# Kernel optimization log

Hardware: AMD Instinct MI355X
Metric: run time of the kernel (lower is better)

Reference implementation:

```python
import jax, jax.numpy as jnp
import numpy as np

EPS = 1e-5


def _prelu(x, a):
    return jnp.where(x >= 0, x, a * x)


def _chan_ln(x, gamma, beta, axis):
    # LayerNormalization4D: normalize over the channel axis, affine per channel
    mu = jnp.mean(x, axis=axis, keepdims=True)
    var = jnp.var(x, axis=axis, keepdims=True)
    return (x - mu) / jnp.sqrt(var + EPS) * gamma + beta


def setup_inputs() -> dict:
    key = jax.random.key(0)
    ks = jax.random.split(key, 12)
    B, C, T, F = 2, 64, 3000, 65
    H, D = 4, 4            # n_head, hid_chan
    E = C // H             # per-head value channels
    s = lambda k, shape: (jax.random.normal(k, shape, jnp.float32) * 0.05)
    return dict(
        x=jax.random.normal(ks[0], (B, C, T, F), jnp.float32),
        # per-head 1x1-conv Q/K/V projections (stacked over head axis)
        Wq=s(ks[1], (H, D, C)), bq=s(ks[2], (H, D)),
        aq=jnp.full((H,), 0.25, jnp.float32),
        gq=jnp.ones((H, D), jnp.float32), betaq=jnp.zeros((H, D), jnp.float32),
        Wk=s(ks[3], (H, D, C)), bk=s(ks[4], (H, D)),
        ak=jnp.full((H,), 0.25, jnp.float32),
        gk=jnp.ones((H, D), jnp.float32), betak=jnp.zeros((H, D), jnp.float32),
        Wv=s(ks[5], (H, E, C)), bv=s(ks[6], (H, E)),
        av=jnp.full((H,), 0.25, jnp.float32),
        gv=jnp.ones((H, E), jnp.float32), betav=jnp.zeros((H, E), jnp.float32),
        # final concat 1x1-conv projection
        Wp=s(ks[7], (C, C)), bp=s(ks[8], (C,)),
        ap=jnp.asarray(0.25, jnp.float32),
        gp=jnp.ones((C,), jnp.float32), betap=jnp.zeros((C,), jnp.float32),
    )


def _conv_act_norm_heads(x, W, b, a, g, beta):
    # x: [B,C,T,F]; W: [H,O,C] -> y: [B,H,O,T,F]
    y = jnp.einsum('hoc,bctf->bhotf', W, x) + b[None, :, :, None, None]
    y = _prelu(y, a[None, :, None, None, None])
    return _chan_ln(y, g[None, :, :, None, None], beta[None, :, :, None, None], axis=2)


def reference(x, Wq, bq, aq, gq, betaq, Wk, bk, ak, gk, betak,
              Wv, bv, av, gv, betav, Wp, bp, ap, gp, betap):
    B, C, T, F = x.shape
    H = Wq.shape[0]
    D = Wq.shape[1]
    E = Wv.shape[1]

    q = _conv_act_norm_heads(x, Wq, bq, aq, gq, betaq)   # [B,H,D,T,F]
    k = _conv_act_norm_heads(x, Wk, bk, ak, gk, betak)   # [B,H,D,T,F]
    v = _conv_act_norm_heads(x, Wv, bv, av, gv, betav)   # [B,H,E,T,F]

    # flatten (chan, freq) -> embedding per time step
    Qf = q.transpose(0, 1, 3, 2, 4).reshape(B, H, T, D * F)
    Kf = k.transpose(0, 1, 3, 2, 4).reshape(B, H, T, D * F)
    Vf = v.transpose(0, 1, 3, 2, 4).reshape(B, H, T, E * F)

    scale = 1.0 / jnp.sqrt(jnp.asarray(D * F, x.dtype))
    attn = jax.nn.softmax(jnp.einsum('bhtd,bhsd->bhts', Qf, Kf) * scale, axis=-1)
    o = jnp.einsum('bhts,bhse->bhte', attn, Vf)          # [B,H,T,E*F]

    # un-flatten and concat heads along channel dim
    o = o.reshape(B, H, T, E, F).transpose(0, 1, 3, 2, 4).reshape(B, H * E, T, F)

    # final 1x1 conv + PReLU + channel LN, then residual
    y = jnp.einsum('oc,bctf->botf', Wp, o) + bp[None, :, None, None]
    y = _prelu(y, ap)
    y = _chan_ln(y, gp[None, :, None, None], betap[None, :, None, None], axis=1)
    return y + x
```

## Files before the change

### kernel.cpp

```cpp
#include <hip/hip_runtime.h>
#include <stdint.h>

#define B_ 2
#define C_ 64
#define T_ 3000
#define F_ 65
#define H_ 4
#define D_ 4
#define E_ 16
#define TF_ (T_*F_)
#define NPT (B_*TF_)
#define EF 1040
#define TP 3072
#define TK 3008
#define DQK 260
#define SQK 328
#define VTROWS 1152
#define ABUF 8192
#define BBUF 4096

typedef unsigned short u16;
typedef unsigned int   u32;
typedef __attribute__((ext_vector_type(8))) short  s16x8;
typedef __attribute__((ext_vector_type(4))) float  f32x4;
typedef __attribute__((ext_vector_type(4))) u32    u32x4;

__device__ __forceinline__ float bf2f(u16 u){ return __uint_as_float(((u32)u)<<16); }
__device__ __forceinline__ float bf2f_lo(u32 u){ return __uint_as_float(u<<16); }
__device__ __forceinline__ float bf2f_hi(u32 u){ return __uint_as_float(u & 0xffff0000u); }
__device__ __forceinline__ u16 f2bf(float f){
  u32 u = __float_as_uint(f);
  u32 r = u + 0x7fffu + ((u>>16)&1u);
  return (u16)(r>>16);
}

__device__ __forceinline__ void gld16(const u16* g, u16* l){
  __builtin_amdgcn_global_load_lds((const __attribute__((address_space(1))) u32*)g,
                                   (__attribute__((address_space(3))) u32*)l,
                                   16, 0, 0);
}

__global__ __launch_bounds__(256) void qkv_kernel(
    const float* __restrict__ x,
    const float* __restrict__ Wq, const float* __restrict__ bq, const float* __restrict__ aq,
    const float* __restrict__ gq, const float* __restrict__ bteq,
    const float* __restrict__ Wk, const float* __restrict__ bk, const float* __restrict__ ak,
    const float* __restrict__ gk, const float* __restrict__ btek,
    const float* __restrict__ Wv, const float* __restrict__ bv, const float* __restrict__ av,
    const float* __restrict__ gv, const float* __restrict__ btev,
    u16* __restrict__ Qf, u16* __restrict__ Kf, u16* __restrict__ Vf,
    float* __restrict__ lbuf)
{
  __shared__ __align__(16) u16 wlds[2*96*64];
  const int tid = threadIdx.x;
  for (int i = tid; i < 6144; i += 256){
    const int row = i >> 6, c = i & 63;
    float w;
    if (row < 16)      w = Wq[row*64 + c];
    else if (row < 32) w = Wk[(row-16)*64 + c];
    else               w = Wv[(row-32)*64 + c];
    const u16 hi = f2bf(w);
    const u16 lo = f2bf(w - bf2f(hi));
    const int byo = ((row<<7) + (c<<1)) ^ ((row&7)<<4);
    *(u16*)((char*)wlds + byo)         = hi;
    *(u16*)((char*)wlds + 12288 + byo) = lo;
  }
  const int gid = blockIdx.x*256 + tid;
  if (gid < 8*TP) lbuf[gid] = 0.f;
  __syncthreads();

  const int wv_ = tid >> 6, l = tid & 63;
  const int lm = l & 15, lq = l >> 4;
  const int p0 = blockIdx.x*128 + wv_*32;

  int bb[2], rr[2]; bool ok[2];
  #pragma unroll
  for (int nt=0; nt<2; nt++){
    int p = p0 + nt*16 + lm;
    ok[nt] = (p < NPT);
    if (p >= NPT) p = NPT-1;
    bb[nt] = (p >= TF_) ? 1 : 0;
    rr[nt] = p - bb[nt]*TF_;
  }

  f32x4 acc[6][2];
  #pragma unroll
  for (int i=0;i<6;i++){
    acc[i][0]=(f32x4){0.f,0.f,0.f,0.f};
    acc[i][1]=(f32x4){0.f,0.f,0.f,0.f};
  }

  #pragma unroll
  for (int ks=0; ks<2; ks++){
    const int c0 = ks*32 + lq*8;
    s16x8 xhi[2], xlo[2];
    #pragma unroll
    for (int nt=0; nt<2; nt++){
      const float* xb = x + ((size_t)bb[nt]*C_ + c0)*TF_ + rr[nt];
      float xr[8];
      #pragma unroll
      for (int j=0;j<8;j++) xr[j] = xb[(size_t)j*TF_];
      u32x4 hw, lw;
      #pragma unroll
      for (int jw=0;jw<4;jw++){
        const u16 h0 = f2bf(xr[jw*2+0]);
        const u16 h1 = f2bf(xr[jw*2+1]);
        const float r0 = xr[jw*2+0] - bf2f(h0);
        const float r1 = xr[jw*2+1] - bf2f(h1);
        hw[jw] = (u32)h0 | ((u32)h1<<16);
        lw[jw] = (u32)f2bf(r0) | ((u32)f2bf(r1)<<16);
      }
      xhi[nt] = __builtin_bit_cast(s16x8, hw);
      xlo[nt] = __builtin_bit_cast(s16x8, lw);
    }
    #pragma unroll
    for (int mt=0; mt<6; mt++){
      const int rowb = mt*16 + lm;
      const int byo = ((rowb<<7) + (c0<<1)) ^ ((rowb&7)<<4);
      const s16x8 whi = *(const s16x8*)((const char*)wlds + byo);
      const s16x8 wlo = *(const s16x8*)((const char*)wlds + 12288 + byo);
      #pragma unroll
      for (int nt=0; nt<2; nt++){
        acc[mt][nt] = __builtin_amdgcn_mfma_f32_16x16x32_bf16(whi, xhi[nt], acc[mt][nt], 0,0,0);
        acc[mt][nt] = __builtin_amdgcn_mfma_f32_16x16x32_bf16(whi, xlo[nt], acc[mt][nt], 0,0,0);
        acc[mt][nt] = __builtin_amdgcn_mfma_f32_16x16x32_bf16(wlo, xhi[nt], acc[mt][nt], 0,0,0);
      }
    }
  }

  #pragma unroll
  for (int nt=0; nt<2; nt++){
    if (!ok[nt]) continue;
    const int b = bb[nt], r = rr[nt];
    const u32 t = (u32)(((unsigned long long)r * 516223ULL) >> 25);
    const int f = r - (int)t*65;
    {
      const int h = lq;
      const float a_ = aq[h];
      float v[4]; float s1 = 0.f;
      #pragma unroll
      for (int d=0; d<4; d++){
        float a = acc[0][nt][d] + bq[h*4+d];
        a = (a >= 0.f) ? a : a_*a;
        v[d] = a; s1 += a;
      }
      const float mu = s1*0.25f;
      float var = 0.f;
      #pragma unroll
      for (int d=0; d<4; d++){ const float dd = v[d]-mu; var = fmaf(dd,dd,var); }
      var *= 0.25f;
      const float rs = rsqrtf(var + 1e-5f);
      u16* qrow = Qf + ((size_t)(b*4+h)*TP + t)*SQK + f;
      #pragma unroll
      for (int d=0; d<4; d++)
        qrow[d*F_] = f2bf((v[d]-mu)*rs*gq[h*4+d] + bteq[h*4+d]);
    }
    {
      const int h = lq;
      const float a_ = ak[h];
      float v[4]; float s1 = 0.f;
      #pragma unroll
      for (int d=0; d<4; d++){
        float a = acc[1][nt][d] + bk[h*4+d];
        a = (a >= 0.f) ? a : a_*a;
        v[d] = a; s1 += a;
      }
      const float mu = s1*0.25f;
      float var = 0.f;
      #pragma unroll
      for (int d=0; d<4; d++){ const float dd = v[d]-mu; var = fmaf(dd,dd,var); }
      var *= 0.25f;
      const float rs = rsqrtf(var + 1e-5f);
      u16* krow = Kf + ((size_t)(b*4+h)*TP + t)*SQK + f;
      #pragma unroll
      for (int d=0; d<4; d++)
        krow[d*F_] = f2bf((v[d]-mu)*rs*gk[h*4+d] + btek[h*4+d]);
    }
    if (f < 28) {
      #pragma unroll
      for (int h2=0; h2<4; h2++){
        Qf[((size_t)(b*4+h2)*TP + t)*SQK + 260 + f] = 0;
        Kf[((size_t)(b*4+h2)*TP + t)*SQK + 260 + f] = 0;
      }
    }
    #pragma unroll
    for (int mt=2; mt<6; mt++){
      const int h = mt-2;
      const float a_ = av[h];
      float v[4]; float s1 = 0.f, s2 = 0.f;
      #pragma unroll
      for (int e4=0; e4<4; e4++){
        float a = acc[mt][nt][e4] + bv[h*16 + lq*4 + e4];
        a = (a >= 0.f) ? a : a_*a;
        v[e4] = a; s1 += a; s2 = fmaf(a,a,s2);
      }
      s1 += __shfl_xor(s1,16); s1 += __shfl_xor(s1,32);
      s2 += __shfl_xor(s2,16); s2 += __shfl_xor(s2,32);
      const float mu = s1*(1.f/16.f);
      const float var = s2*(1.f/16.f) - mu*mu;
      const float rs = rsqrtf(var + 1e-5f);
      u16* vrow = Vf + ((size_t)(b*4+h)*T_ + t)*EF + f;
      #pragma unroll
      for (int e4=0; e4<4; e4++){
        const int e = lq*4 + e4;
        vrow[e*F_] = f2bf((v[e4]-mu)*rs*gv[h*16+e] + btev[h*16+e]);
      }
    }
  }
}

__global__ __launch_bounds__(256) void vtrans_kernel(
    const u16* __restrict__ Vf, u16* __restrict__ Vt)
{
  __shared__ u16 tile[64][68];
  const int bh = blockIdx.z, t0 = blockIdx.x*64, c0 = blockIdx.y*64;
  const int tid = threadIdx.x;
  const int rr = tid>>4, cc4 = (tid&15)*4;
  #pragma unroll
  for (int i=0;i<4;i++){
    const int key = t0 + rr + i*16;
    ushort4 v = {0,0,0,0};
    if (key < T_) {
      const u16* src = Vf + ((size_t)bh*T_ + key)*EF + c0 + cc4;
      if (c0 + cc4 + 3 < EF) v = *(const ushort4*)src;
      else {
        if (c0+cc4+0 < EF) v.x = src[0];
        if (c0+cc4+1 < EF) v.y = src[1];
        if (c0+cc4+2 < EF) v.z = src[2];
        if (c0+cc4+3 < EF) v.w = src[3];
      }
    }
    *(ushort4*)&tile[rr + i*16][cc4] = v;
  }
  __syncthreads();
  #pragma unroll
  for (int i=0;i<4;i++){
    const int cl = rr + i*16;
    const int col = c0 + cl;
    ushort4 v;
    v.x = tile[cc4+0][cl];
    v.y = tile[cc4+1][cl];
    v.z = tile[cc4+2][cl];
    v.w = tile[cc4+3][cl];
    *(ushort4*)(Vt + ((size_t)bh*VTROWS + col)*TK + t0 + cc4) = v;
  }
}

__device__ __forceinline__ void gemm_core(
    const u16* __restrict__ Ag, const u16* __restrict__ Bg,
    size_t strideA, size_t strideB, int niter,
    u16* As, u16* Bs, f32x4 acc[4][4], int w, int l, int tid)
{
  const int sa1 = tid + 512;
  const int ra0 = tid>>2, ja0 = (tid&3) ^ ((ra0>>1)&3);
  const int ra1 = sa1>>2, ja1 = (sa1&3) ^ ((ra1>>1)&3);
  const int jb0 = (tid&3) ^ ((ra0>>1)&3);
  const u16* gA0 = Ag + (size_t)ra0*strideA + ja0*8;
  const u16* gA1 = Ag + (size_t)ra1*strideA + ja1*8;
  const u16* gB0 = Bg + (size_t)ra0*strideB + jb0*8;
  u16* lA0 = As + (size_t)(w*64)*8;
  u16* lA1 = As + (size_t)(512 + w*64)*8;
  u16* lB0 = Bs + (size_t)(w*64)*8;
  const int m = l & 15, q = l >> 4;
  const int sw = (q ^ ((m>>1)&3)) << 3;
  const int ra = (w&3)*64 + m;
  const int rb = (w>>2)*64 + m;

  #pragma unroll
  for (int t=0; t<3; ++t){
    if (t < niter){
      const int k0 = t*32;
      gld16(gA0 + k0, lA0 + t*ABUF);
      gld16(gA1 + k0, lA1 + t*ABUF);
      gld16(gB0 + k0, lB0 + t*BBUF);
    }
  }
  int cur = 0;
  for (int it = 0; it < niter; ++it) {
    if (it < niter-2)      asm volatile("s_waitcnt vmcnt(6)" ::: "memory");
    else if (it < niter-1) asm volatile("s_waitcnt vmcnt(3)" ::: "memory");
    else                   asm volatile("s_waitcnt vmcnt(0)" ::: "memory");
    __builtin_amdgcn_s_barrier();
    __builtin_amdgcn_sched_barrier(0);
    s16x8 a[4], b[4];
    #pragma unroll
    for (int i=0;i<4;i++) a[i] = *(const s16x8*)(As + cur*ABUF + (ra + i*16)*32 + sw);
    #pragma unroll
    for (int j=0;j<4;j++) b[j] = *(const s16x8*)(Bs + cur*BBUF + (rb + j*16)*32 + sw);
    #pragma unroll
    for (int i=0;i<4;i++)
      #pragma unroll
      for (int j=0;j<4;j++)
        acc[i][j] = __builtin_amdgcn_mfma_f32_16x16x32_bf16(a[i], b[j], acc[i][j], 0, 0, 0);
    __builtin_amdgcn_sched_barrier(0);
    __builtin_amdgcn_s_barrier();
    if (it + 3 < niter) {
      const int k0 = (it+3)*32;
      gld16(gA0 + k0, lA0 + cur*ABUF);
      gld16(gA1 + k0, lA1 + cur*ABUF);
      gld16(gB0 + k0, lB0 + cur*BBUF);
    }
    cur = (cur == 2) ? 0 : cur + 1;
  }
}

__global__ __launch_bounds__(512) void scores_kernel(
    const u16* __restrict__ Qf, const u16* __restrict__ Kf,
    u16* __restrict__ P, float* __restrict__ lbuf, int bh0)
{
  __shared__ __align__(16) u16 As[3*ABUF];
  __shared__ __align__(16) u16 Bs[3*BBUF];
  const int tid = threadIdx.x, w = tid>>6, l = tid&63;
  const int bh = bh0 + blockIdx.z;
  const int gcol0 = blockIdx.x*256, row0 = blockIdx.y*128;
  const u16* Ag = Kf + ((size_t)bh*TP + gcol0)*SQK;
  const u16* Bg = Qf + ((size_t)bh*TP + row0)*SQK;

  f32x4 acc[4][4];
  #pragma unroll
  for (int i=0;i<4;i++)
    #pragma unroll
    for (int j=0;j<4;j++) acc[i][j] = (f32x4){0.f,0.f,0.f,0.f};

  gemm_core(Ag, Bg, SQK, SQK, 9, As, Bs, acc, w, l, tid);

  const float scale = 0.062017367294604234f;
  const int m = l & 15, q = l >> 4;
  u16* Pz = P + (size_t)blockIdx.z*TP*TP;
  float* lrow = lbuf + (size_t)bh*TP;

  float rsum[4] = {0.f,0.f,0.f,0.f};
  #pragma unroll
  for (int i=0;i<4;i++){
    const int gcb = gcol0 + (w&3)*64 + i*16 + q*4;
    #pragma unroll
    for (int j=0;j<4;j++){
      const int grow = row0 + (w>>2)*64 + j*16 + m;
      float pv[4];
      #pragma unroll
      for (int reg=0; reg<4; reg++){
        float v = __expf(acc[i][j][reg]*scale);
        if (gcb + reg >= T_) v = 0.f;
        pv[reg] = v; rsum[j] += v;
      }
      const u32 lo = (u32)f2bf(pv[0]) | ((u32)f2bf(pv[1])<<16);
      const u32 hi = (u32)f2bf(pv[2]) | ((u32)f2bf(pv[3])<<16);
      *(uint2*)(Pz + (size_t)grow*TP + gcb) = make_uint2(lo, hi);
    }
  }
  #pragma unroll
  for (int j=0;j<4;j++){
    float r = rsum[j];
    r += __shfl_xor(r, 16);
    r += __shfl_xor(r, 32);
    if (q == 0) atomicAdd(&lrow[row0 + (w>>2)*64 + j*16 + m], r);
  }
}

__global__ __launch_bounds__(512) void pv_kernel(
    const u16* __restrict__ P, const u16* __restrict__ Vt,
    const float* __restrict__ lbuf, u16* __restrict__ Og, int bh0)
{
  __shared__ __align__(16) u16 As[3*ABUF];
  __shared__ __align__(16) u16 Bs[3*BBUF];
  const int tid = threadIdx.x, w = tid>>6, l = tid&63;
  const int bh = bh0 + blockIdx.z;
  const int row0 = blockIdx.x*256, col0 = blockIdx.y*128;
  const u16* Ag = P + (size_t)blockIdx.z*TP*TP + (size_t)row0*TP;
  const u16* Bg = Vt + ((size_t)bh*VTROWS + col0)*TK;

  f32x4 acc[4][4];
  #pragma unroll
  for (int i=0;i<4;i++)
    #pragma unroll
    for (int j=0;j<4;j++) acc[i][j] = (f32x4){0.f,0.f,0.f,0.f};

  gemm_core(Ag, Bg, TP, TK, 94, As, Bs, acc, w, l, tid);

  const int m = l & 15, q = l >> 4;
  const float* lrow = lbuf + (size_t)bh*TP;

  #pragma unroll
  for (int i=0;i<4;i++){
    #pragma unroll
    for (int reg=0; reg<4; reg++){
      const int grow = row0 + (w&3)*64 + i*16 + q*4 + reg;
      if (grow >= T_) continue;
      const float linv = 1.0f / lrow[grow];
      u16* orow = Og + ((size_t)bh*T_ + grow)*EF;
      #pragma unroll
      for (int j=0;j<4;j++){
        const int gcol = col0 + (w>>2)*64 + j*16 + m;
        if (gcol < EF)
          orow[gcol] = f2bf(acc[i][j][reg]*linv);
      }
    }
  }
}

__global__ __launch_bounds__(256) void outp_kernel(
    const u16* __restrict__ Og, const float* __restrict__ x,
    const float* __restrict__ Wp, const float* __restrict__ bp, const float* __restrict__ ap,
    const float* __restrict__ gp, const float* __restrict__ btep,
    float* __restrict__ out)
{
  __shared__ __align__(16) u16 wlds[2*64*64];
  __shared__ float prm[193];
  const int tid = threadIdx.x;
  for (int i = tid; i < 4096; i += 256){
    const int row = i >> 6, c = i & 63;
    const float w = Wp[row*64 + c];
    const u16 hi = f2bf(w);
    const u16 lo = f2bf(w - bf2f(hi));
    const int byo = ((row<<7) + (c<<1)) ^ ((row&7)<<4);
    *(u16*)((char*)wlds + byo)        = hi;
    *(u16*)((char*)wlds + 8192 + byo) = lo;
  }
  if (tid < 193) {
    float v;
    if      (tid < 64)  v = bp[tid];
    else if (tid < 128) v = gp[tid-64];
    else if (tid < 192) v = btep[tid-128];
    else                v = ap[0];
    prm[tid] = v;
  }
  __syncthreads();

  const int wv_ = tid >> 6, l = tid & 63;
  const int lm = l & 15, lq = l >> 4;
  const int p0 = blockIdx.x*128 + wv_*32;

  int bb[2], rr[2], tt[2], ff[2]; bool ok[2];
  #pragma unroll
  for (int nt=0; nt<2; nt++){
    int p = p0 + nt*16 + lm;
    ok[nt] = (p < NPT);
    if (p >= NPT) p = NPT-1;
    bb[nt] = (p >= TF_) ? 1 : 0;
    rr[nt] = p - bb[nt]*TF_;
    tt[nt] = (int)(((unsigned long long)rr[nt] * 516223ULL) >> 25);
    ff[nt] = rr[nt] - tt[nt]*65;
  }

  f32x4 acc[4][2];
  #pragma unroll
  for (int i=0;i<4;i++){
    acc[i][0]=(f32x4){0.f,0.f,0.f,0.f};
    acc[i][1]=(f32x4){0.f,0.f,0.f,0.f};
  }

  #pragma unroll
  for (int ks=0; ks<2; ks++){
    const int c0 = ks*32 + lq*8;
    const int h  = c0 >> 4;
    const int e0 = c0 & 15;
    s16x8 xf[2];
    #pragma unroll
    for (int nt=0; nt<2; nt++){
      const u16* base = Og + ((size_t)(bb[nt]*4 + h)*T_ + tt[nt])*EF + ff[nt];
      u32x4 pk;
      #pragma unroll
      for (int jw=0; jw<4; jw++){
        const u16 v0 = base[(e0 + jw*2 + 0)*65];
        const u16 v1 = base[(e0 + jw*2 + 1)*65];
        pk[jw] = (u32)v0 | ((u32)v1 << 16);
      }
      xf[nt] = __builtin_bit_cast(s16x8, pk);
    }
    #pragma unroll
    for (int mt=0; mt<4; mt++){
      const int rowb = mt*16 + lm;
      const int byo = ((rowb<<7) + (c0<<1)) ^ ((rowb&7)<<4);
      const s16x8 whi = *(const s16x8*)((const char*)wlds + byo);
      const s16x8 wlo = *(const s16x8*)((const char*)wlds + 8192 + byo);
      #pragma unroll
      for (int nt=0; nt<2; nt++){
        acc[mt][nt] = __builtin_amdgcn_mfma_f32_16x16x32_bf16(whi, xf[nt], acc[mt][nt], 0,0,0);
        acc[mt][nt] = __builtin_amdgcn_mfma_f32_16x16x32_bf16(wlo, xf[nt], acc[mt][nt], 0,0,0);
      }
    }
  }

  const float apv = prm[192];
  #pragma unroll
  for (int nt=0; nt<2; nt++){
    if (!ok[nt]) continue;
    const int b = bb[nt], r = rr[nt];
    float v[4][4]; float s1 = 0.f, s2 = 0.f;
    #pragma unroll
    for (int mt=0; mt<4; mt++){
      #pragma unroll
      for (int reg=0; reg<4; reg++){
        const int o = mt*16 + lq*4 + reg;
        float a = acc[mt][nt][reg] + prm[o];
        a = (a >= 0.f) ? a : apv*a;
        v[mt][reg] = a; s1 += a; s2 = fmaf(a,a,s2);
      }
    }
    s1 += __shfl_xor(s1,16); s1 += __shfl_xor(s1,32);
    s2 += __shfl_xor(s2,16); s2 += __shfl_xor(s2,32);
    const float mu = s1*(1.f/64.f);
    const float var = s2*(1.f/64.f) - mu*mu;
    const float rs = rsqrtf(var + 1e-5f);
    const float* xb = x + (size_t)b*C_*TF_ + r;
    float* yb = out + (size_t)b*C_*TF_ + r;
    #pragma unroll
    for (int mt=0; mt<4; mt++){
      #pragma unroll
      for (int reg=0; reg<4; reg++){
        const int o = mt*16 + lq*4 + reg;
        yb[(size_t)o*TF_] = fmaf((v[mt][reg]-mu)*rs, prm[64+o], prm[128+o]) + xb[(size_t)o*TF_];
      }
    }
  }
}

extern "C" void kernel_launch(void* const* d_in, const int* in_sizes, int n_in,
                              void* d_out, int out_size, void* d_ws, size_t ws_size,
                              hipStream_t stream)
{
  const float* x    = (const float*)d_in[0];
  const float* Wq   = (const float*)d_in[1];
  const float* bq   = (const float*)d_in[2];
  const float* aq   = (const float*)d_in[3];
  const float* gq   = (const float*)d_in[4];
  const float* bteq = (const float*)d_in[5];
  const float* Wk   = (const float*)d_in[6];
  const float* bk   = (const float*)d_in[7];
  const float* ak   = (const float*)d_in[8];
  const float* gk   = (const float*)d_in[9];
  const float* btek = (const float*)d_in[10];
  const float* Wv   = (const float*)d_in[11];
  const float* bv   = (const float*)d_in[12];
  const float* av   = (const float*)d_in[13];
  const float* gv   = (const float*)d_in[14];
  const float* btev = (const float*)d_in[15];
  const float* Wp   = (const float*)d_in[16];
  const float* bp   = (const float*)d_in[17];
  const float* ap   = (const float*)d_in[18];
  const float* gp   = (const float*)d_in[19];
  const float* btep = (const float*)d_in[20];

  char* ws = (char*)d_ws;
  u16*   Qf   = (u16*)(ws + 0);
  u16*   Kf   = (u16*)(ws + 16121856);
  u16*   Vf   = (u16*)(ws + 32243712);
  u16*   Og   = (u16*)(ws + 32243712);
  u16*   Vt   = (u16*)(ws + 82163712);
  const bool z4 = (ws_size >= (size_t)213202944);
  u16*   P;
  float* lbuf;
  if (z4) { lbuf = (float*)(ws + 137607168); P = (u16*)(ws + 137705472); }
  else    { P = (u16*)(ws + 137607168);      lbuf = (float*)(ws + 175355904); }
  float* out  = (float*)d_out;

  qkv_kernel<<<dim3((NPT+127)/128), dim3(256), 0, stream>>>(
      x, Wq,bq,aq,gq,bteq, Wk,bk,ak,gk,btek, Wv,bv,av,gv,btev, Qf,Kf,Vf, lbuf);
  vtrans_kernel<<<dim3(47, 17, 8), dim3(256), 0, stream>>>(Vf, Vt);
  if (z4) {
    for (int c = 0; c < 2; ++c) {
      scores_kernel<<<dim3(12, 24, 4), dim3(512), 0, stream>>>(Qf, Kf, P, lbuf, c*4);
      pv_kernel<<<dim3(12, 9, 4), dim3(512), 0, stream>>>(P, Vt, lbuf, Og, c*4);
    }
  } else {
    for (int c = 0; c < 4; ++c) {
      scores_kernel<<<dim3(12, 24, 2), dim3(512), 0, stream>>>(Qf, Kf, P, lbuf, c*2);
      pv_kernel<<<dim3(12, 9, 2), dim3(512), 0, stream>>>(P, Vt, lbuf, Og, c*2);
    }
  }
  outp_kernel<<<dim3((NPT+127)/128), dim3(256), 0, stream>>>(
      Og, x, Wp,bp,ap,gp,btep, out);
}
```

Before: 684.6 us.

## Interleave channel and frequency in Q/K/V/O layouts for vectorized access

Changes the flattened embedding order from channel-major (d*F+f) to frequency-major (f*D+d) for Q, K, V and the attention output. Each thread can then pack its four bf16 outputs into one 8-byte store instead of four strided 2-byte stores. The final projection loads its 8 channels as a single 16-byte vector instead of eight strided gathers. This works because the attention dot products and the PV product are invariant to a consistent permutation of the embedding dimension, but every consumer must agree on the new order.

After: 691.3 us. No clear change (+1.0%).

```diff
diff --git a/kernel.cpp b/kernel.cpp
--- a/kernel.cpp
+++ b/kernel.cpp
@@ -150,10 +150,13 @@
       for (int d=0; d<4; d++){ const float dd = v[d]-mu; var = fmaf(dd,dd,var); }
       var *= 0.25f;
       const float rs = rsqrtf(var + 1e-5f);
-      u16* qrow = Qf + ((size_t)(b*4+h)*TP + t)*SQK + f;
+      u16 o[4];
       #pragma unroll
       for (int d=0; d<4; d++)
-        qrow[d*F_] = f2bf((v[d]-mu)*rs*gq[h*4+d] + bteq[h*4+d]);
+        o[d] = f2bf((v[d]-mu)*rs*gq[h*4+d] + bteq[h*4+d]);
+      const u32 lo = (u32)o[0] | ((u32)o[1]<<16);
+      const u32 hi = (u32)o[2] | ((u32)o[3]<<16);
+      *(uint2*)(Qf + ((size_t)(b*4+h)*TP + t)*SQK + f*4) = make_uint2(lo, hi);
     }
     {
       const int h = lq;
@@ -171,10 +174,13 @@
       for (int d=0; d<4; d++){ const float dd = v[d]-mu; var = fmaf(dd,dd,var); }
       var *= 0.25f;
       const float rs = rsqrtf(var + 1e-5f);
-      u16* krow = Kf + ((size_t)(b*4+h)*TP + t)*SQK + f;
+      u16 o[4];
       #pragma unroll
       for (int d=0; d<4; d++)
-        krow[d*F_] = f2bf((v[d]-mu)*rs*gk[h*4+d] + btek[h*4+d]);
+        o[d] = f2bf((v[d]-mu)*rs*gk[h*4+d] + btek[h*4+d]);
+      const u32 lo = (u32)o[0] | ((u32)o[1]<<16);
+      const u32 hi = (u32)o[2] | ((u32)o[3]<<16);
+      *(uint2*)(Kf + ((size_t)(b*4+h)*TP + t)*SQK + f*4) = make_uint2(lo, hi);
     }
     if (f < 28) {
       #pragma unroll
@@ -199,12 +205,15 @@
       const float mu = s1*(1.f/16.f);
       const float var = s2*(1.f/16.f) - mu*mu;
       const float rs = rsqrtf(var + 1e-5f);
-      u16* vrow = Vf + ((size_t)(b*4+h)*T_ + t)*EF + f;
+      u16 o[4];
       #pragma unroll
       for (int e4=0; e4<4; e4++){
         const int e = lq*4 + e4;
-        vrow[e*F_] = f2bf((v[e4]-mu)*rs*gv[h*16+e] + btev[h*16+e]);
-      }
+        o[e4] = f2bf((v[e4]-mu)*rs*gv[h*16+e] + btev[h*16+e]);
+      }
+      const u32 lo = (u32)o[0] | ((u32)o[1]<<16);
+      const u32 hi = (u32)o[2] | ((u32)o[3]<<16);
+      *(uint2*)(Vf + ((size_t)(b*4+h)*T_ + t)*EF + f*16 + lq*4) = make_uint2(lo, hi);
     }
   }
 }
@@ -457,15 +466,8 @@
     s16x8 xf[2];
     #pragma unroll
     for (int nt=0; nt<2; nt++){
-      const u16* base = Og + ((size_t)(bb[nt]*4 + h)*T_ + tt[nt])*EF + ff[nt];
-      u32x4 pk;
-      #pragma unroll
-      for (int jw=0; jw<4; jw++){
-        const u16 v0 = base[(e0 + jw*2 + 0)*65];
-        const u16 v1 = base[(e0 + jw*2 + 1)*65];
-        pk[jw] = (u32)v0 | ((u32)v1 << 16);
-      }
-      xf[nt] = __builtin_bit_cast(s16x8, pk);
+      const u16* base = Og + ((size_t)(bb[nt]*4 + h)*T_ + tt[nt])*EF + ff[nt]*16 + e0;
+      xf[nt] = *(const s16x8*)base;
     }
     #pragma unroll
     for (int mt=0; mt<4; mt++){
```
